# Kernel optimization log

Hardware: AMD Instinct MI355X
Metric: run time of the kernel (lower is better)

Reference implementation:

```python
import jax, jax.numpy as jnp
import numpy as np

B, T, C, H = 2, 2048, 1024, 16
D = C // H  # head dim = 64


def setup_inputs() -> dict:
    key = jax.random.key(0)
    ks = jax.random.split(key, 5)
    s = 0.02
    return {
        "x": jax.random.normal(ks[0], (B, T, C), dtype=jnp.float32),
        "c_attn_w": jax.random.normal(ks[1], (C, 3 * C), dtype=jnp.float32) * s,
        "c_attn_b": jax.random.normal(ks[2], (3 * C,), dtype=jnp.float32) * s,
        "c_proj_w": jax.random.normal(ks[3], (C, C), dtype=jnp.float32) * s,
        "c_proj_b": jax.random.normal(ks[4], (C,), dtype=jnp.float32) * s,
    }


def reference(x, c_attn_w, c_attn_b, c_proj_w, c_proj_b):
    b, t, c = x.shape
    # GPT-2 Conv1D: x @ W + b
    qkv = x @ c_attn_w + c_attn_b                      # [B,T,3C]
    q, k, v = jnp.split(qkv, 3, axis=-1)
    # [B,H,T,D]
    q = q.reshape(b, t, H, D).transpose(0, 2, 1, 3)
    k = k.reshape(b, t, H, D).transpose(0, 2, 1, 3)
    v = v.reshape(b, t, H, D).transpose(0, 2, 1, 3)
    scale = 1.0 / jnp.sqrt(jnp.float32(D))
    scores = jnp.einsum("bhqd,bhkd->bhqk", q, k) * scale  # [B,H,T,T]
    causal = jnp.tril(jnp.ones((t, t), dtype=bool))
    scores = jnp.where(causal, scores, jnp.float32(-jnp.inf))
    attn = jax.nn.softmax(scores, axis=-1)
    # drop_rate = 0.0 -> dropout is identity
    y = jnp.einsum("bhqk,bhkd->bhqd", attn, v)          # [B,H,T,D]
    y = y.transpose(0, 2, 1, 3).reshape(b, t, c)
    return y @ c_proj_w + c_proj_b
```

## Files before the change

kernel.cpp:

```cpp
#include <hip/hip_runtime.h>

#define B_ 2
#define T_ 2048
#define C_ 1024
#define H_ 16
#define D_ 64
#define M_ (B_ * T_)
#define NQKV_ (3 * C_)

typedef unsigned short us16;
typedef short bf16x8 __attribute__((ext_vector_type(8)));
typedef float f32x4 __attribute__((ext_vector_type(4)));

__device__ __forceinline__ f32x4 mfma16(bf16x8 a, bf16x8 b, f32x4 c) {
    return __builtin_amdgcn_mfma_f32_16x16x32_bf16(a, b, c, 0, 0, 0);
}

__device__ __forceinline__ us16 f2bf(float f) {
    union { float f; unsigned int u; } v; v.f = f;
    unsigned int r = v.u + 0x7fffu + ((v.u >> 16) & 1u);
    return (us16)(r >> 16);
}

__device__ __forceinline__ void gl_lds16(const us16* g, us16* l) {
    __builtin_amdgcn_global_load_lds(
        (const __attribute__((address_space(1))) void*)g,
        (__attribute__((address_space(3))) void*)l,
        16, 0, 0);
}

__global__ __launch_bounds__(256) void cvt_bf16(
    const float* __restrict__ in, us16* __restrict__ out, int n8)
{
    const int i = blockIdx.x * blockDim.x + threadIdx.x;
    if (i >= n8) return;
    const float4 a = ((const float4*)in)[2 * i];
    const float4 b = ((const float4*)in)[2 * i + 1];
    ushort4 lo = { f2bf(a.x), f2bf(a.y), f2bf(a.z), f2bf(a.w) };
    ushort4 hi = { f2bf(b.x), f2bf(b.y), f2bf(b.z), f2bf(b.w) };
    ((ushort4*)out)[2 * i] = lo;
    ((ushort4*)out)[2 * i + 1] = hi;
}

__global__ __launch_bounds__(256) void transpose_cvt(
    const float* __restrict__ W, us16* __restrict__ Wt, int K, int N)
{
    __shared__ float tile[32][33];
    const int n0 = blockIdx.x * 32, k0 = blockIdx.y * 32;
    const int t = threadIdx.x;
    {
        const int k = t >> 3, n4 = (t & 7) * 4;
        const float4 v = *(const float4*)(W + (size_t)(k0 + k) * N + n0 + n4);
        tile[k][n4 + 0] = v.x; tile[k][n4 + 1] = v.y;
        tile[k][n4 + 2] = v.z; tile[k][n4 + 3] = v.w;
    }
    __syncthreads();
    {
        const int n = t >> 3, k4 = (t & 7) * 4;
        ushort4 o = { f2bf(tile[k4 + 0][n]), f2bf(tile[k4 + 1][n]),
                      f2bf(tile[k4 + 2][n]), f2bf(tile[k4 + 3][n]) };
        *(ushort4*)(Wt + (size_t)(n0 + n) * K + k0 + k4) = o;
    }
}

__global__ __launch_bounds__(256) void gemm_bf16(
    const us16* __restrict__ A, const us16* __restrict__ Bt,
    const float* __restrict__ bias, void* __restrict__ Cout,
    int M, int N, int K, int out_bf16)
{
    __shared__ __align__(16) us16 smem[128 * 136];
    us16* sA = smem;
    us16* sB = smem + 128 * 64;

    const int tid = threadIdx.x;
    const int lane = tid & 63, wave = tid >> 6;
    const int wr = wave >> 1, wc = wave & 1;
    const int cq = lane & 15, quad = lane >> 4;
    const int m0 = blockIdx.y * 128, n0 = blockIdx.x * 128;

    const int srow  = lane >> 3;
    const int sgran = (lane & 7) ^ srow;
    const int scol  = sgran * 8;

    f32x4 acc[4][4];
    #pragma unroll
    for (int i = 0; i < 4; ++i)
        #pragma unroll
        for (int j = 0; j < 4; ++j)
            acc[i][j] = (f32x4){0.f, 0.f, 0.f, 0.f};

    for (int k0 = 0; k0 < K; k0 += 64) {
        #pragma unroll
        for (int p = 0; p < 4; ++p) {
            const int r = p * 32 + wave * 8;
            gl_lds16(A  + (size_t)(m0 + r + srow) * K + k0 + scol, sA + r * 64);
            gl_lds16(Bt + (size_t)(n0 + r + srow) * K + k0 + scol, sB + r * 64);
        }
        __syncthreads();

        #pragma unroll
        for (int kk = 0; kk < 64; kk += 32) {
            const int koS = (((kk >> 3) + quad) ^ (cq & 7)) << 3;
            bf16x8 af[4], bfg[4];
            #pragma unroll
            for (int i = 0; i < 4; ++i) {
                af[i]  = *(const bf16x8*)(sA + (wr * 64 + i * 16 + cq) * 64 + koS);
                bfg[i] = *(const bf16x8*)(sB + (wc * 64 + i * 16 + cq) * 64 + koS);
            }
            #pragma unroll
            for (int mi = 0; mi < 4; ++mi)
                #pragma unroll
                for (int ni = 0; ni < 4; ++ni)
                    acc[mi][ni] = mfma16(af[mi], bfg[ni], acc[mi][ni]);
        }
        __syncthreads();
    }

    if (out_bf16) {
        us16* Cs = smem;
        #pragma unroll
        for (int mi = 0; mi < 4; ++mi)
            #pragma unroll
            for (int ni = 0; ni < 4; ++ni) {
                const int n = n0 + wc * 64 + ni * 16 + cq;
                const float bv = bias[n];
                #pragma unroll
                for (int r = 0; r < 4; ++r)
                    Cs[(wr * 64 + mi * 16 + quad * 4 + r) * 136 +
                       wc * 64 + ni * 16 + cq] = f2bf(acc[mi][ni][r] + bv);
            }
        __syncthreads();
        us16* Co = (us16*)Cout;
        #pragma unroll
        for (int p = 0; p < 8; ++p) {
            const int chunk = p * 256 + tid;
            const int r = chunk >> 4, c = (chunk & 15) * 8;
            *(uint4*)(Co + (size_t)(m0 + r) * N + n0 + c) =
                *(const uint4*)(Cs + r * 136 + c);
        }
    } else {
        float* Co = (float*)Cout;
        #pragma unroll
        for (int mi = 0; mi < 4; ++mi)
            #pragma unroll
            for (int ni = 0; ni < 4; ++ni) {
                const int n = n0 + wc * 64 + ni * 16 + cq;
                const float bv = bias[n];
                #pragma unroll
                for (int r = 0; r < 4; ++r)
                    Co[(size_t)(m0 + wr * 64 + mi * 16 + quad * 4 + r) * N + n] =
                        acc[mi][ni][r] + bv;
            }
    }
}

__global__ __launch_bounds__(256) void attn_mfma(
    const us16* __restrict__ qkv, us16* __restrict__ y,
    float* __restrict__ Pp, float* __restrict__ lp)
{
    __shared__ __align__(16) us16 Ks[64][72];
    __shared__ __align__(16) us16 Vt[64][72];
    __shared__ __align__(16) us16 Ps[64][72];

    const int tid = threadIdx.x;
    const int lane = tid & 63, wave = tid >> 6;
    const int cq = lane & 15, quad = lane >> 4;
    const int bh = blockIdx.x;
    const int j = blockIdx.y;
    const int b = bh >> 4, h = bh & 15;

    int qt, k0t, k1t, slot;
    if (j < 4)       { qt = 19 - j;        k0t = 0;  k1t = qt; slot = -1; }
    else if (j < 16) { qt = 31 - (j - 4);  const int lo = (qt + 2) >> 1;
                       k0t = 0;  k1t = lo - 1; slot = (31 - qt) * 2; }
    else if (j < 28) { qt = 31 - (j - 16); const int lo = (qt + 2) >> 1;
                       k0t = lo; k1t = qt; slot = (31 - qt) * 2 + 1; }
    else             { qt = 43 - j;        k0t = 0;  k1t = qt; slot = -1; }

    const us16* base = qkv + (size_t)b * T_ * NQKV_ + h * D_;

    bf16x8 qf[2];
    {
        const us16* qrow = base + (size_t)(qt * 64 + wave * 16 + cq) * NQKV_;
        qf[0] = *(const bf16x8*)(qrow + quad * 8);
        qf[1] = *(const bf16x8*)(qrow + 32 + quad * 8);
    }

    f32x4 ot[4];
    #pragma unroll
    for (int jj = 0; jj < 4; ++jj) ot[jj] = (f32x4){0.f, 0.f, 0.f, 0.f};
    f32x4 os = (f32x4){0.f, 0.f, 0.f, 0.f};

    const bf16x8 onesf = (bf16x8){16256, 16256, 16256, 16256,
                                  16256, 16256, 16256, 16256};

    const float ESCL = 0.125f;
    const float ESH  = -3.0f;

    const int kr0 = tid >> 3;
    const int kr1 = (256 + tid) >> 3;
    const int kc8 = (tid & 7) * 8;
    const int t2 = tid & 31, dc = tid >> 5;

    const us16* Kg = base + C_;
    const us16* Vg = base + 2 * C_;

    uint4 ka0 = *(const uint4*)(Kg + ((size_t)k0t * 64 + kr0) * NQKV_ + kc8);
    uint4 ka1 = *(const uint4*)(Kg + ((size_t)k0t * 64 + kr1) * NQKV_ + kc8);
    uint4 va0, va1;
    {
        const us16* vp = Vg + ((size_t)k0t * 64 + 2 * t2) * NQKV_ + dc * 8;
        va0 = *(const uint4*)vp;
        va1 = *(const uint4*)(vp + NQKV_);
    }

    for (int kt = k0t; kt <= k1t; ++kt) {
        *(uint4*)(&Ks[kr0][kc8]) = ka0;
        *(uint4*)(&Ks[kr1][kc8]) = ka1;
        {
            const us16* p0 = (const us16*)&va0;
            const us16* p1 = (const us16*)&va1;
            #pragma unroll
            for (int jj = 0; jj < 8; ++jj) {
                const unsigned int packed =
                    (unsigned int)p0[jj] | ((unsigned int)p1[jj] << 16);
                *(unsigned int*)(&Vt[dc * 8 + jj][2 * t2]) = packed;
            }
        }
        __syncthreads();

        if (kt < k1t) {
            const size_t ro = (size_t)((kt + 1) * 64);
            ka0 = *(const uint4*)(Kg + (ro + kr0) * NQKV_ + kc8);
            ka1 = *(const uint4*)(Kg + (ro + kr1) * NQKV_ + kc8);
            const us16* vp = Vg + (ro + 2 * t2) * NQKV_ + dc * 8;
            va0 = *(const uint4*)vp;
            va1 = *(const uint4*)(vp + NQKV_);
        }

        f32x4 s[4];
        #pragma unroll
        for (int jj = 0; jj < 4; ++jj) {
            const bf16x8 kf0 = *(const bf16x8*)(&Ks[jj * 16 + cq][quad * 8]);
            const bf16x8 kf1 = *(const bf16x8*)(&Ks[jj * 16 + cq][32 + quad * 8]);
            f32x4 t = (f32x4){0.f, 0.f, 0.f, 0.f};
            t = mfma16(qf[0], kf0, t);
            t = mfma16(qf[1], kf1, t);
            s[jj] = t;
        }

        float p[4][4];
        if (kt == qt) {
            const int qloc = wave * 16 + quad * 4;
            #pragma unroll
            for (int jj = 0; jj < 4; ++jj) {
                const int kloc = jj * 16 + cq;
                #pragma unroll
                for (int r = 0; r < 4; ++r) {
                    const float e = __expf(fmaf(s[jj][r], ESCL, ESH));
                    p[jj][r] = (kloc > qloc + r) ? 0.f : e;
                }
            }
        } else {
            #pragma unroll
            for (int jj = 0; jj < 4; ++jj)
                #pragma unroll
                for (int r = 0; r < 4; ++r)
                    p[jj][r] = __expf(fmaf(s[jj][r], ESCL, ESH));
        }

        #pragma unroll
        for (int jj = 0; jj < 4; ++jj)
            #pragma unroll
            for (int r = 0; r < 4; ++r) {
                union { float f; unsigned int u; } cv; cv.f = p[jj][r];
                Ps[wave * 16 + quad * 4 + r][jj * 16 + cq] =
                    (us16)(cv.u >> 16);
            }

        const bf16x8 pf0 = *(const bf16x8*)(&Ps[wave * 16 + cq][quad * 8]);
        const bf16x8 pf1 = *(const bf16x8*)(&Ps[wave * 16 + cq][32 + quad * 8]);

        os = mfma16(onesf, pf0, os);
        os = mfma16(onesf, pf1, os);
        #pragma unroll
        for (int dt = 0; dt < 4; ++dt) {
            const bf16x8 vf0 = *(const bf16x8*)(&Vt[dt * 16 + cq][quad * 8]);
            const bf16x8 vf1 = *(const bf16x8*)(&Vt[dt * 16 + cq][32 + quad * 8]);
            ot[dt] = mfma16(vf0, pf0, ot[dt]);
            ot[dt] = mfma16(vf1, pf1, ot[dt]);
        }

        __syncthreads();
    }

    if (slot >= 0) {
        const int sg = bh * 24 + slot;
        float* Pb = Pp + (size_t)sg * 4096;
        #pragma unroll
        for (int dt = 0; dt < 4; ++dt)
            #pragma unroll
            for (int i = 0; i < 4; ++i)
                Pb[(dt * 16 + quad * 4 + i) * 64 + wave * 16 + cq] = ot[dt][i];
        if (quad == 0) lp[(size_t)sg * 64 + wave * 16 + cq] = os[0];
    } else {
        const float inv = 1.0f / os[0];
        const int row = qt * 64 + wave * 16 + cq;
        us16* yp = y + (size_t)(b * T_ + row) * C_ + h * D_ + quad * 4;
        #pragma unroll
        for (int dt = 0; dt < 4; ++dt) {
            ushort4 ov = { f2bf(ot[dt][0] * inv), f2bf(ot[dt][1] * inv),
                           f2bf(ot[dt][2] * inv), f2bf(ot[dt][3] * inv) };
            *(ushort4*)(yp + dt * 16) = ov;
        }
    }
}

__global__ __launch_bounds__(256) void attn_combine(
    const float* __restrict__ Pp, const float* __restrict__ lp,
    us16* __restrict__ y)
{
    const int bh = blockIdx.x, si = blockIdx.y;
    const int qt = 31 - si;
    const int b = bh >> 4, h = bh & 15;
    const int t = threadIdx.x;
    const int q = t & 63, dg = t >> 6;

    const size_t sgA = (size_t)bh * 24 + si * 2;
    const float la = lp[sgA * 64 + q];
    const float lb = lp[(sgA + 1) * 64 + q];
    const float inv = 1.0f / (la + lb);
    const float* PA = Pp + sgA * 4096;
    const float* PB = PA + 4096;

    __align__(16) us16 ob[16];
    #pragma unroll
    for (int i = 0; i < 16; ++i) {
        const int d = dg * 16 + i;
        ob[i] = f2bf((PA[d * 64 + q] + PB[d * 64 + q]) * inv);
    }
    us16* yp = y + (size_t)(b * T_ + qt * 64 + q) * C_ + h * D_ + dg * 16;
    *(uint4*)(yp)     = *(const uint4*)(&ob[0]);
    *(uint4*)(yp + 8) = *(const uint4*)(&ob[8]);
}

extern "C" void kernel_launch(void* const* d_in, const int* in_sizes, int n_in,
                              void* d_out, int out_size, void* d_ws, size_t ws_size,
                              hipStream_t stream)
{
    const float* x  = (const float*)d_in[0];
    const float* aw = (const float*)d_in[1];
    const float* ab = (const float*)d_in[2];
    const float* pw = (const float*)d_in[3];
    const float* pb = (const float*)d_in[4];
    float* out = (float*)d_out;

    us16* xb   = (us16*)d_ws;
    us16* awT  = xb  + (size_t)M_ * C_;
    us16* pwT  = awT + (size_t)NQKV_ * C_;
    us16* qkvb = pwT + (size_t)C_ * C_;
    us16* yb   = qkvb + (size_t)M_ * NQKV_;

    float* Pp = (float*)d_ws;
    float* lp = Pp + (size_t)768 * 4096;

    cvt_bf16<<<(M_ * C_ / 8 + 255) / 256, 256, 0, stream>>>(x, xb, M_ * C_ / 8);
    transpose_cvt<<<dim3(NQKV_ / 32, C_ / 32), 256, 0, stream>>>(aw, awT, C_, NQKV_);
    transpose_cvt<<<dim3(C_ / 32, C_ / 32), 256, 0, stream>>>(pw, pwT, C_, C_);

    gemm_bf16<<<dim3(NQKV_ / 128, M_ / 128), 256, 0, stream>>>(
        xb, awT, ab, qkvb, M_, NQKV_, C_, 1);

    attn_mfma<<<dim3(B_ * H_, 44), 256, 0, stream>>>(qkvb, yb, Pp, lp);
    attn_combine<<<dim3(B_ * H_, 12), 256, 0, stream>>>(Pp, lp, yb);

    gemm_bf16<<<dim3(C_ / 128, M_ / 128), 256, 0, stream>>>(
        yb, pwT, pb, out, M_, C_, C_, 0);
}
```

Before: 198.1 us.

## Split-K the output projection GEMM and add a bf16 partial-sum combine kernel

The c_proj GEMM now runs with two K-splits in gridDim.z, which doubles the block count from 256 to 512 so more of the GPU's compute units stay busy. Each split writes bf16 partials into the reused qkv buffer, and a new elementwise kernel adds the two partials plus the bias into the fp32 output. In exchange it adds a kernel launch and extra memory traffic, and rounding the partials to bf16 loses some precision compared with the fp32 output the projection wrote before.

```diff
diff --git a/kernel.cpp b/kernel.cpp
--- a/kernel.cpp
+++ b/kernel.cpp
@@ -20,6 +20,11 @@
     union { float f; unsigned int u; } v; v.f = f;
     unsigned int r = v.u + 0x7fffu + ((v.u >> 16) & 1u);
     return (us16)(r >> 16);
+}
+
+__device__ __forceinline__ float bf2f(us16 u) {
+    union { unsigned int u; float f; } v; v.u = (unsigned int)u << 16;
+    return v.f;
 }
 
 __device__ __forceinline__ void gl_lds16(const us16* g, us16* l) {
@@ -66,7 +71,7 @@
 __global__ __launch_bounds__(256) void gemm_bf16(
     const us16* __restrict__ A, const us16* __restrict__ Bt,
     const float* __restrict__ bias, void* __restrict__ Cout,
-    int M, int N, int K, int out_bf16)
+    int M, int N, int K, int out_mode)
 {
     __shared__ __align__(16) us16 smem[128 * 136];
     us16* sA = smem;
@@ -78,6 +83,10 @@
     const int cq = lane & 15, quad = lane >> 4;
     const int m0 = blockIdx.y * 128, n0 = blockIdx.x * 128;
 
+    const int kz = blockIdx.z;
+    const int klen = K / (int)gridDim.z;
+    const int kbeg = kz * klen;
+
     const int srow  = lane >> 3;
     const int sgran = (lane & 7) ^ srow;
     const int scol  = sgran * 8;
@@ -89,7 +98,7 @@
         for (int j = 0; j < 4; ++j)
             acc[i][j] = (f32x4){0.f, 0.f, 0.f, 0.f};
 
-    for (int k0 = 0; k0 < K; k0 += 64) {
+    for (int k0 = kbeg; k0 < kbeg + klen; k0 += 64) {
         #pragma unroll
         for (int p = 0; p < 4; ++p) {
             const int r = p * 32 + wave * 8;
@@ -116,21 +125,22 @@
         __syncthreads();
     }
 
-    if (out_bf16) {
+    if (out_mode) {
+        const bool with_bias = (out_mode == 1);
         us16* Cs = smem;
         #pragma unroll
         for (int mi = 0; mi < 4; ++mi)
             #pragma unroll
             for (int ni = 0; ni < 4; ++ni) {
                 const int n = n0 + wc * 64 + ni * 16 + cq;
-                const float bv = bias[n];
+                const float bv = with_bias ? bias[n] : 0.f;
                 #pragma unroll
                 for (int r = 0; r < 4; ++r)
                     Cs[(wr * 64 + mi * 16 + quad * 4 + r) * 136 +
                        wc * 64 + ni * 16 + cq] = f2bf(acc[mi][ni][r] + bv);
             }
         __syncthreads();
-        us16* Co = (us16*)Cout;
+        us16* Co = (us16*)Cout + (size_t)kz * M * N;
         #pragma unroll
         for (int p = 0; p < 8; ++p) {
             const int chunk = p * 256 + tid;
@@ -154,6 +164,32 @@
     }
 }
 
+__global__ __launch_bounds__(256) void gemm2_combine(
+    const us16* __restrict__ P, const float* __restrict__ bias,
+    float* __restrict__ out)
+{
+    const int i = blockIdx.x * blockDim.x + threadIdx.x;
+    const size_t e = (size_t)i * 8;
+    const int c = (int)(e & (C_ - 1));
+    const us16* p0 = P + e;
+    const us16* p1 = P + (size_t)M_ * C_ + e;
+    const ushort4 a0 = *(const ushort4*)p0, a1 = *(const ushort4*)(p0 + 4);
+    const ushort4 b0 = *(const ushort4*)p1, b1 = *(const ushort4*)(p1 + 4);
+    const float4 bl = *(const float4*)(bias + c);
+    const float4 bh = *(const float4*)(bias + c + 4);
+    float4 o0, o1;
+    o0.x = bf2f(a0.x) + bf2f(b0.x) + bl.x;
+    o0.y = bf2f(a0.y) + bf2f(b0.y) + bl.y;
+    o0.z = bf2f(a0.z) + bf2f(b0.z) + bl.z;
+    o0.w = bf2f(a0.w) + bf2f(b0.w) + bl.w;
+    o1.x = bf2f(a1.x) + bf2f(b1.x) + bh.x;
+    o1.y = bf2f(a1.y) + bf2f(b1.y) + bh.y;
+    o1.z = bf2f(a1.z) + bf2f(b1.z) + bh.z;
+    o1.w = bf2f(a1.w) + bf2f(b1.w) + bh.w;
+    *(float4*)(out + e)     = o0;
+    *(float4*)(out + e + 4) = o1;
+}
+
 __global__ __launch_bounds__(256) void attn_mfma(
     const us16* __restrict__ qkv, us16* __restrict__ y,
     float* __restrict__ Pp, float* __restrict__ lp)
@@ -363,6 +399,7 @@
 
     float* Pp = (float*)d_ws;
     float* lp = Pp + (size_t)768 * 4096;
+    us16* g2p = qkvb;
 
     cvt_bf16<<<(M_ * C_ / 8 + 255) / 256, 256, 0, stream>>>(x, xb, M_ * C_ / 8);
     transpose_cvt<<<dim3(NQKV_ / 32, C_ / 32), 256, 0, stream>>>(aw, awT, C_, NQKV_);
@@ -374,6 +411,7 @@
     attn_mfma<<<dim3(B_ * H_, 44), 256, 0, stream>>>(qkvb, yb, Pp, lp);
     attn_combine<<<dim3(B_ * H_, 12), 256, 0, stream>>>(Pp, lp, yb);
 
-    gemm_bf16<<<dim3(C_ / 128, M_ / 128), 256, 0, stream>>>(
-        yb, pwT, pb, out, M_, C_, C_, 0);
-}
+    gemm_bf16<<<dim3(C_ / 128, M_ / 128, 2), 256, 0, stream>>>(
+        yb, pwT, pb, g2p, M_, C_, C_, 2);
+    gemm2_combine<<<(M_ * C_ / 8) / 256, 256, 0, stream>>>(g2p, pb, out);
+}
```

New measurement: 195.3 us. About the same (-1.4%).
